# Kernel tuning notes

Measured on AMD Instinct MI355X. Metric: run time of the kernel, lower is better.

The kernel has to match this reference:

```python
import jax, jax.numpy as jnp
import numpy as np

B, D, H, P, NH = 16384, 4096, 32, 16, 32
S = H - P  # num_sub_layer = 16
TAU = 5.0
NEG = -1e9


def setup_inputs() -> dict:
    key = jax.random.key(0)
    k1, k2, k3, k4, k5 = jax.random.split(key, 5)
    x = jax.random.normal(k1, (B, D), jnp.float32)
    latency = jax.random.uniform(k2, (B,), jnp.float32)  # fraction in [0,1); clamped later
    W_head = jax.random.normal(k3, (D, S), jnp.float32) * 0.02
    b_head = jax.random.normal(k4, (S,), jnp.float32) * 0.02
    # pre-drawn gumbel noise for up to S sampling rounds: [S, B, S]
    u = jax.random.uniform(k5, (S, B, S), jnp.float32, minval=1e-6, maxval=1.0 - 1e-6)
    gumbel = -jnp.log(-jnp.log(u))
    return {"x": x, "latency": latency, "W_head": W_head, "b_head": b_head, "gumbel": gumbel}


def reference(x, latency, W_head, b_head, gumbel):
    # latency_quantizing: number of sub-layers to execute per sample
    n = jnp.clip(jnp.round(latency * H), P, H) - P  # [B] float in [0, S]
    logits = x @ W_head + b_head                    # [B, S]

    # n-times hard gumbel-softmax without replacement, vectorized over batch.
    def step(mask, inp):
        g, t = inp                                   # g: [B,S] gumbel noise, t: step index
        masked = logits + mask * NEG                 # exclude already-selected layers
        soft = jax.nn.softmax((masked + g) / TAU, axis=-1)
        hard = jax.nn.one_hot(jnp.argmax(soft, axis=-1), S, dtype=soft.dtype)
        sample = soft + jax.lax.stop_gradient(hard - soft)  # straight-through
        active = (t < n)[:, None]                    # per-sample variable draw count
        return mask + jnp.where(active, sample, 0.0), None

    ts = jnp.arange(S, dtype=jnp.float32)
    mask, _ = jax.lax.scan(step, jnp.zeros_like(logits), (gumbel, ts))  # [B, S] multi-hot

    # [B, S] -> [B, S, 2, NH]
    out = jnp.broadcast_to(mask[:, :, None, None], (mask.shape[0], S, 2, NH))
    prefix = jnp.ones((mask.shape[0], P, 2, NH), mask.dtype)  # prefix layers always run
    return jnp.concatenate([prefix, out], axis=1)             # [B, H, 2, NH]
```

## Files before the change

### kernel.cpp

```cpp
#include <hip/hip_runtime.h>


#define BB 16384
#define DD 4096

typedef float f32x4 __attribute__((ext_vector_type(4)));

__global__ __launch_bounds__(512, 2) void simple_scheduler_kernel(
    const float* __restrict__ x, const float* __restrict__ lat,
    const float* __restrict__ W, const float* __restrict__ bh,
    const float* __restrict__ gum, float* __restrict__ out) {
  __shared__ float smem[8 * 2112];

  const int t = threadIdx.x;
  const int lane = t & 63;
  const int wid = __builtin_amdgcn_readfirstlane(t >> 6);
  const int rb = blockIdx.x * 64;

  float a0[16], a1[16], a2[16], a3[16];
#pragma unroll
  for (int j = 0; j < 16; ++j) { a0[j] = 0.f; a1[j] = 0.f; a2[j] = 0.f; a3[j] = 0.f; }

  const int k0 = wid * 512;
  float* tile = smem + wid * 2112;
  const int r8 = lane >> 3;
  const int c4 = (lane & 7) * 4;
  const int lrow = lane * 33;
  const float* xbase = x + (size_t)(rb + r8) * DD + k0 + c4;

  f32x4 v[8];
#pragma unroll
  for (int rr = 0; rr < 8; ++rr)
    v[rr] = __builtin_nontemporal_load(
        reinterpret_cast<const f32x4*>(xbase + (size_t)rr * 8 * DD));

  for (int s = 0; s < 16; ++s) {
    const int kc = k0 + s * 32;
#pragma unroll
    for (int rr = 0; rr < 8; ++rr) {
      const int o = (r8 + rr * 8) * 33 + c4;
      tile[o] = v[rr].x; tile[o + 1] = v[rr].y;
      tile[o + 2] = v[rr].z; tile[o + 3] = v[rr].w;
    }
    if (s < 15) {
      const float* xn = xbase + (s + 1) * 32;
#pragma unroll
      for (int rr = 0; rr < 8; ++rr)
        v[rr] = __builtin_nontemporal_load(
            reinterpret_cast<const f32x4*>(xn + (size_t)rr * 8 * DD));
    }
#pragma unroll
    for (int i = 0; i < 32; i += 4) {
      const float x0 = tile[lrow + i];
      const float x1 = tile[lrow + i + 1];
      const float x2 = tile[lrow + i + 2];
      const float x3 = tile[lrow + i + 3];
      const float* w0 = W + (size_t)(kc + i) * 16;
#pragma unroll
      for (int j = 0; j < 16; ++j) {
        a0[j] = fmaf(w0[j],      x0, a0[j]);
        a1[j] = fmaf(w0[16 + j], x1, a1[j]);
        a2[j] = fmaf(w0[32 + j], x2, a2[j]);
        a3[j] = fmaf(w0[48 + j], x3, a3[j]);
      }
    }
  }

  __syncthreads();
  float* red    = smem;
  float* logitl = smem + 8704;
  float* selb   = smem + 9792;

#pragma unroll
  for (int j = 0; j < 16; ++j)
    red[wid * 1088 + lane * 17 + j] = (a0[j] + a1[j]) + (a2[j] + a3[j]);
  __syncthreads();

  {
    int p = t;
#pragma unroll
    for (int rep = 0; rep < 2; ++rep, p += 512) {
      const int row = p >> 4, j = p & 15;
      float ssum = 0.f;
#pragma unroll
      for (int w = 0; w < 8; ++w) ssum += red[w * 1088 + row * 17 + j];
      logitl[row * 17 + j] = ssum + bh[j];
    }
  }
  __syncthreads();

  f32x4* op = reinterpret_cast<f32x4*>(out + (size_t)rb * 2048);

  if (t >= 64) {
    const f32x4 ones = {1.f, 1.f, 1.f, 1.f};
    for (int i = t - 64; i < 64 * 256; i += 448) {
      const int row = i >> 8, col = i & 255;
      __builtin_nontemporal_store(ones, &op[(size_t)row * 512 + col]);
    }
  } else {
    const int row = rb + lane;
    float lg[16];
#pragma unroll
    for (int j = 0; j < 16; ++j) lg[j] = logitl[lane * 17 + j];

    float nf = rintf(lat[row] * 32.0f);
    nf = fminf(fmaxf(nf, 16.0f), 32.0f);
    const int n = (int)nf - 16;

    int nmax = n;
#pragma unroll
    for (int o = 32; o > 0; o >>= 1) nmax = max(nmax, __shfl_xor(nmax, o));

    unsigned sel = 0u;
    for (int tt = 0; tt < nmax; ++tt) {
      if (tt < n) {
        const float* gp = gum + ((size_t)tt * BB + row) * 16;
        const f32x4 g0 = reinterpret_cast<const f32x4*>(gp)[0];
        const f32x4 g1 = reinterpret_cast<const f32x4*>(gp)[1];
        const f32x4 g2 = reinterpret_cast<const f32x4*>(gp)[2];
        const f32x4 g3 = reinterpret_cast<const f32x4*>(gp)[3];
        const float gv[16] = {g0.x, g0.y, g0.z, g0.w, g1.x, g1.y, g1.z, g1.w,
                              g2.x, g2.y, g2.z, g2.w, g3.x, g3.y, g3.z, g3.w};
        float av[16];
#pragma unroll
        for (int j = 0; j < 16; ++j) {
          const float masked = lg[j] + (((sel >> j) & 1u) ? -1e9f : 0.0f);
          av[j] = (masked + gv[j]) / 5.0f;
        }
        float m = av[0];
#pragma unroll
        for (int j = 1; j < 16; ++j) m = fmaxf(m, av[j]);
        float ev[16];
        float se = 0.f;
#pragma unroll
        for (int j = 0; j < 16; ++j) { ev[j] = expf(av[j] - m); se += ev[j]; }
        float pm = ev[0] / se;
        int jm = 0;
#pragma unroll
        for (int j = 1; j < 16; ++j) {
          const float pj = ev[j] / se;
          if (pj > pm) { pm = pj; jm = j; }
        }
        sel |= 1u << jm;
      }
    }
#pragma unroll
    for (int j = 0; j < 16; ++j)
      selb[lane * 17 + j] = ((sel >> j) & 1u) ? 1.0f : 0.0f;
  }
  __syncthreads();

  for (int i = t; i < 64 * 256; i += 512) {
    const int row = i >> 8, c = i & 255;
    const float vv = selb[row * 17 + (c >> 4)];
    const f32x4 vvv = {vv, vv, vv, vv};
    __builtin_nontemporal_store(vvv, &op[(size_t)row * 512 + 256 + c]);
  }
}

extern "C" void kernel_launch(void* const* d_in, const int* in_sizes, int n_in,
                              void* d_out, int out_size, void* d_ws, size_t ws_size,
                              hipStream_t stream) {
  const float* x   = (const float*)d_in[0];
  const float* lat = (const float*)d_in[1];
  const float* W   = (const float*)d_in[2];
  const float* bh  = (const float*)d_in[3];
  const float* gum = (const float*)d_in[4];
  float* out = (float*)d_out;

  const int B = in_sizes[1];
  simple_scheduler_kernel<<<B / 64, 512, 0, stream>>>(x, lat, W, bh, gum, out);
}
```

Measured before the change: 442.7 us.

## Double-buffer x register prefetch and software-pipeline gumbel loads in sampling loop

The GEMV main loop now keeps two register buffers of x so loads are issued two stages ahead instead of one, giving more memory-level parallelism to hide global load latency. The gumbel-softmax sampling loop prefetches the next round's noise while computing the current round. The cost is higher register pressure (16 more f32x4 values), which under launch_bounds(512,2) could cause spills or lower occupancy.

```diff
diff --git a/kernel.cpp b/kernel.cpp
--- a/kernel.cpp
+++ b/kernel.cpp
@@ -28,43 +28,49 @@
   const int lrow = lane * 33;
   const float* xbase = x + (size_t)(rb + r8) * DD + k0 + c4;
 
-  f32x4 v[8];
+  f32x4 va[8], vb[8];
 #pragma unroll
-  for (int rr = 0; rr < 8; ++rr)
-    v[rr] = __builtin_nontemporal_load(
+  for (int rr = 0; rr < 8; ++rr) {
+    va[rr] = __builtin_nontemporal_load(
         reinterpret_cast<const f32x4*>(xbase + (size_t)rr * 8 * DD));
+    vb[rr] = __builtin_nontemporal_load(
+        reinterpret_cast<const f32x4*>(xbase + (size_t)rr * 8 * DD + 32));
+  }
 
-  for (int s = 0; s < 16; ++s) {
-    const int kc = k0 + s * 32;
-#pragma unroll
-    for (int rr = 0; rr < 8; ++rr) {
-      const int o = (r8 + rr * 8) * 33 + c4;
-      tile[o] = v[rr].x; tile[o + 1] = v[rr].y;
-      tile[o + 2] = v[rr].z; tile[o + 3] = v[rr].w;
-    }
-    if (s < 15) {
-      const float* xn = xbase + (s + 1) * 32;
-#pragma unroll
-      for (int rr = 0; rr < 8; ++rr)
-        v[rr] = __builtin_nontemporal_load(
-            reinterpret_cast<const f32x4*>(xn + (size_t)rr * 8 * DD));
-    }
-#pragma unroll
-    for (int i = 0; i < 32; i += 4) {
-      const float x0 = tile[lrow + i];
-      const float x1 = tile[lrow + i + 1];
-      const float x2 = tile[lrow + i + 2];
-      const float x3 = tile[lrow + i + 3];
-      const float* w0 = W + (size_t)(kc + i) * 16;
-#pragma unroll
-      for (int j = 0; j < 16; ++j) {
-        a0[j] = fmaf(w0[j],      x0, a0[j]);
-        a1[j] = fmaf(w0[16 + j], x1, a1[j]);
-        a2[j] = fmaf(w0[32 + j], x2, a2[j]);
-        a3[j] = fmaf(w0[48 + j], x3, a3[j]);
-      }
-    }
+#define STAGE_BODY(s, VCUR)                                                   \
+  {                                                                           \
+    const int kc = k0 + (s) * 32;                                             \
+    _Pragma("unroll") for (int rr = 0; rr < 8; ++rr) {                        \
+      const int o = (r8 + rr * 8) * 33 + c4;                                  \
+      tile[o] = VCUR[rr].x; tile[o + 1] = VCUR[rr].y;                         \
+      tile[o + 2] = VCUR[rr].z; tile[o + 3] = VCUR[rr].w;                     \
+    }                                                                         \
+    if ((s) < 14) {                                                           \
+      const float* xn = xbase + ((s) + 2) * 32;                               \
+      _Pragma("unroll") for (int rr = 0; rr < 8; ++rr)                        \
+        VCUR[rr] = __builtin_nontemporal_load(                                \
+            reinterpret_cast<const f32x4*>(xn + (size_t)rr * 8 * DD));        \
+    }                                                                         \
+    _Pragma("unroll") for (int i = 0; i < 32; i += 4) {                       \
+      const float x0 = tile[lrow + i];                                        \
+      const float x1 = tile[lrow + i + 1];                                    \
+      const float x2 = tile[lrow + i + 2];                                    \
+      const float x3 = tile[lrow + i + 3];                                    \
+      const float* w0 = W + (size_t)(kc + i) * 16;                            \
+      _Pragma("unroll") for (int j = 0; j < 16; ++j) {                        \
+        a0[j] = fmaf(w0[j],      x0, a0[j]);                                  \
+        a1[j] = fmaf(w0[16 + j], x1, a1[j]);                                  \
+        a2[j] = fmaf(w0[32 + j], x2, a2[j]);                                  \
+        a3[j] = fmaf(w0[48 + j], x3, a3[j]);                                  \
+      }                                                                       \
+    }                                                                         \
   }
+
+  for (int s = 0; s < 16; s += 2) {
+    STAGE_BODY(s, va);
+    STAGE_BODY(s + 1, vb);
+  }
+#undef STAGE_BODY
 
   __syncthreads();
   float* red    = smem;
@@ -112,36 +118,47 @@
     for (int o = 32; o > 0; o >>= 1) nmax = max(nmax, __shfl_xor(nmax, o));
 
     unsigned sel = 0u;
-    for (int tt = 0; tt < nmax; ++tt) {
-      if (tt < n) {
-        const float* gp = gum + ((size_t)tt * BB + row) * 16;
-        const f32x4 g0 = reinterpret_cast<const f32x4*>(gp)[0];
-        const f32x4 g1 = reinterpret_cast<const f32x4*>(gp)[1];
-        const f32x4 g2 = reinterpret_cast<const f32x4*>(gp)[2];
-        const f32x4 g3 = reinterpret_cast<const f32x4*>(gp)[3];
-        const float gv[16] = {g0.x, g0.y, g0.z, g0.w, g1.x, g1.y, g1.z, g1.w,
-                              g2.x, g2.y, g2.z, g2.w, g3.x, g3.y, g3.z, g3.w};
-        float av[16];
+    if (nmax > 0) {
+      const float* gb = gum + (size_t)row * 16;
+      f32x4 g0 = reinterpret_cast<const f32x4*>(gb)[0];
+      f32x4 g1 = reinterpret_cast<const f32x4*>(gb)[1];
+      f32x4 g2 = reinterpret_cast<const f32x4*>(gb)[2];
+      f32x4 g3 = reinterpret_cast<const f32x4*>(gb)[3];
+      for (int tt = 0; tt < nmax; ++tt) {
+        f32x4 h0, h1, h2, h3;
+        if (tt + 1 < nmax) {
+          const float* gp = gb + ((size_t)(tt + 1) * BB) * 16;
+          h0 = reinterpret_cast<const f32x4*>(gp)[0];
+          h1 = reinterpret_cast<const f32x4*>(gp)[1];
+          h2 = reinterpret_cast<const f32x4*>(gp)[2];
+          h3 = reinterpret_cast<const f32x4*>(gp)[3];
+        }
+        if (tt < n) {
+          const float gv[16] = {g0.x, g0.y, g0.z, g0.w, g1.x, g1.y, g1.z, g1.w,
+                                g2.x, g2.y, g2.z, g2.w, g3.x, g3.y, g3.z, g3.w};
+          float av[16];
 #pragma unroll
-        for (int j = 0; j < 16; ++j) {
-          const float masked = lg[j] + (((sel >> j) & 1u) ? -1e9f : 0.0f);
-          av[j] = (masked + gv[j]) / 5.0f;
+          for (int j = 0; j < 16; ++j) {
+            const float masked = lg[j] + (((sel >> j) & 1u) ? -1e9f : 0.0f);
+            av[j] = (masked + gv[j]) / 5.0f;
+          }
+          float m = av[0];
+#pragma unroll
+          for (int j = 1; j < 16; ++j) m = fmaxf(m, av[j]);
+          float ev[16];
+          float se = 0.f;
+#pragma unroll
+          for (int j = 0; j < 16; ++j) { ev[j] = expf(av[j] - m); se += ev[j]; }
+          float pm = ev[0] / se;
+          int jm = 0;
+#pragma unroll
+          for (int j = 1; j < 16; ++j) {
+            const float pj = ev[j] / se;
+            if (pj > pm) { pm = pj; jm = j; }
+          }
+          sel |= 1u << jm;
         }
-        float m = av[0];
-#pragma unroll
-        for (int j = 1; j < 16; ++j) m = fmaxf(m, av[j]);
-        float ev[16];
-        float se = 0.f;
-#pragma unroll
-        for (int j = 0; j < 16; ++j) { ev[j] = expf(av[j] - m); se += ev[j]; }
-        float pm = ev[0] / se;
-        int jm = 0;
-#pragma unroll
-        for (int j = 1; j < 16; ++j) {
-          const float pj = ev[j] / se;
-          if (pj > pm) { pm = pj; jm = j; }
-        }
-        sel |= 1u << jm;
+        g0 = h0; g1 = h1; g2 = h2; g3 = h3;
       }
     }
 #pragma unroll
```

Result: slower. 501.1 us (+13.2%).

## Double block to 1024 threads, split K-slices across wave pairs, prefetch gumbel rows

Applied to the files above, without the earlier changes.

Each block now runs 16 waves instead of 8. Pairs of waves share a 512-wide K slice, each handling two of every four columns with float2 loads, and the reduction sums 16 partial buffers. This halves accumulator registers per thread, raises the number of loads in flight and aims to hide x-stream latency better. The gumbel sampling loop also prefetches the next step's noise row ahead of the softmax compute. In exchange, x loads become narrower 8-byte accesses and the cross-wave reduction gets longer.

```diff
diff --git a/kernel.cpp b/kernel.cpp
--- a/kernel.cpp
+++ b/kernel.cpp
@@ -5,87 +5,87 @@
 #define DD 4096
 
 typedef float f32x4 __attribute__((ext_vector_type(4)));
+typedef float f32x2 __attribute__((ext_vector_type(2)));
 
-__global__ __launch_bounds__(512, 2) void simple_scheduler_kernel(
+__global__ __launch_bounds__(1024, 4) void simple_scheduler_kernel(
     const float* __restrict__ x, const float* __restrict__ lat,
     const float* __restrict__ W, const float* __restrict__ bh,
     const float* __restrict__ gum, float* __restrict__ out) {
-  __shared__ float smem[8 * 2112];
+  __shared__ float smem[16 * 1088];
 
   const int t = threadIdx.x;
   const int lane = t & 63;
   const int wid = __builtin_amdgcn_readfirstlane(t >> 6);
   const int rb = blockIdx.x * 64;
 
-  float a0[16], a1[16], a2[16], a3[16];
+  const int kpart = wid & 7;
+  const int k0 = kpart * 512;
+  const int hs = (wid >= 8) ? 2 : 0;
+
+  float a0[16], a1[16];
 #pragma unroll
-  for (int j = 0; j < 16; ++j) { a0[j] = 0.f; a1[j] = 0.f; a2[j] = 0.f; a3[j] = 0.f; }
+  for (int j = 0; j < 16; ++j) { a0[j] = 0.f; a1[j] = 0.f; }
 
-  const int k0 = wid * 512;
-  float* tile = smem + wid * 2112;
+  float* tile = smem + wid * 1088;
   const int r8 = lane >> 3;
-  const int c4 = (lane & 7) * 4;
-  const int lrow = lane * 33;
-  const float* xbase = x + (size_t)(rb + r8) * DD + k0 + c4;
+  const int c = lane & 7;
+  const int lrow = lane * 17;
+  const float* xbase = x + (size_t)(rb + r8) * DD + k0 + 4 * c + hs;
+  const float* wbase = W + hs * 16;
 
-  f32x4 v[8];
+  f32x2 v[8];
 #pragma unroll
   for (int rr = 0; rr < 8; ++rr)
     v[rr] = __builtin_nontemporal_load(
-        reinterpret_cast<const f32x4*>(xbase + (size_t)rr * 8 * DD));
+        reinterpret_cast<const f32x2*>(xbase + (size_t)rr * 8 * DD));
 
   for (int s = 0; s < 16; ++s) {
-    const int kc = k0 + s * 32;
 #pragma unroll
     for (int rr = 0; rr < 8; ++rr) {
-      const int o = (r8 + rr * 8) * 33 + c4;
+      const int o = (r8 + rr * 8) * 17 + 2 * c;
       tile[o] = v[rr].x; tile[o + 1] = v[rr].y;
-      tile[o + 2] = v[rr].z; tile[o + 3] = v[rr].w;
     }
     if (s < 15) {
       const float* xn = xbase + (s + 1) * 32;
 #pragma unroll
       for (int rr = 0; rr < 8; ++rr)
         v[rr] = __builtin_nontemporal_load(
-            reinterpret_cast<const f32x4*>(xn + (size_t)rr * 8 * DD));
+            reinterpret_cast<const f32x2*>(xn + (size_t)rr * 8 * DD));
     }
 #pragma unroll
-    for (int i = 0; i < 32; i += 4) {
-      const float x0 = tile[lrow + i];
-      const float x1 = tile[lrow + i + 1];
-      const float x2 = tile[lrow + i + 2];
-      const float x3 = tile[lrow + i + 3];
-      const float* w0 = W + (size_t)(kc + i) * 16;
+    for (int i = 0; i < 8; ++i) {
+      const float x0 = tile[lrow + 2 * i];
+      const float x1 = tile[lrow + 2 * i + 1];
+      const float* w0 = wbase + (size_t)(k0 + s * 32 + 4 * i) * 16;
 #pragma unroll
       for (int j = 0; j < 16; ++j) {
         a0[j] = fmaf(w0[j],      x0, a0[j]);
         a1[j] = fmaf(w0[16 + j], x1, a1[j]);
-        a2[j] = fmaf(w0[32 + j], x2, a2[j]);
-        a3[j] = fmaf(w0[48 + j], x3, a3[j]);
       }
     }
   }
 
   __syncthreads();
-  float* red    = smem;
-  float* logitl = smem + 8704;
-  float* selb   = smem + 9792;
+  float* red = smem;
 
 #pragma unroll
   for (int j = 0; j < 16; ++j)
-    red[wid * 1088 + lane * 17 + j] = (a0[j] + a1[j]) + (a2[j] + a3[j]);
+    red[wid * 1088 + lane * 17 + j] = a0[j] + a1[j];
   __syncthreads();
 
+  float* logitl = smem;
+  float* selb   = smem + 1088;
   {
-    int p = t;
+    const int row = t >> 4, j = t & 15;
+    float ssum = 0.f;
 #pragma unroll
-    for (int rep = 0; rep < 2; ++rep, p += 512) {
-      const int row = p >> 4, j = p & 15;
-      float ssum = 0.f;
-#pragma unroll
-      for (int w = 0; w < 8; ++w) ssum += red[w * 1088 + row * 17 + j];
-      logitl[row * 17 + j] = ssum + bh[j];
+    for (int w = 0; w < 8; ++w) {
+      const float pr = red[w * 1088 + row * 17 + j] +
+                       red[(w + 8) * 1088 + row * 17 + j];
+      ssum += pr;
     }
+    const float lv = ssum + bh[j];
+    logitl[row * 17 + j] = lv;
   }
   __syncthreads();
 
@@ -93,7 +93,7 @@
 
   if (t >= 64) {
     const f32x4 ones = {1.f, 1.f, 1.f, 1.f};
-    for (int i = t - 64; i < 64 * 256; i += 448) {
+    for (int i = t - 64; i < 64 * 256; i += 960) {
       const int row = i >> 8, col = i & 255;
       __builtin_nontemporal_store(ones, &op[(size_t)row * 512 + col]);
     }
@@ -112,36 +112,47 @@
     for (int o = 32; o > 0; o >>= 1) nmax = max(nmax, __shfl_xor(nmax, o));
 
     unsigned sel = 0u;
-    for (int tt = 0; tt < nmax; ++tt) {
-      if (tt < n) {
-        const float* gp = gum + ((size_t)tt * BB + row) * 16;
-        const f32x4 g0 = reinterpret_cast<const f32x4*>(gp)[0];
-        const f32x4 g1 = reinterpret_cast<const f32x4*>(gp)[1];
-        const f32x4 g2 = reinterpret_cast<const f32x4*>(gp)[2];
-        const f32x4 g3 = reinterpret_cast<const f32x4*>(gp)[3];
-        const float gv[16] = {g0.x, g0.y, g0.z, g0.w, g1.x, g1.y, g1.z, g1.w,
-                              g2.x, g2.y, g2.z, g2.w, g3.x, g3.y, g3.z, g3.w};
-        float av[16];
+    if (nmax > 0) {
+      const float* gb = gum + (size_t)row * 16;
+      f32x4 g0 = reinterpret_cast<const f32x4*>(gb)[0];
+      f32x4 g1 = reinterpret_cast<const f32x4*>(gb)[1];
+      f32x4 g2 = reinterpret_cast<const f32x4*>(gb)[2];
+      f32x4 g3 = reinterpret_cast<const f32x4*>(gb)[3];
+      for (int tt = 0; tt < nmax; ++tt) {
+        f32x4 h0, h1, h2, h3;
+        if (tt + 1 < nmax) {
+          const float* gp = gb + ((size_t)(tt + 1) * BB) * 16;
+          h0 = reinterpret_cast<const f32x4*>(gp)[0];
+          h1 = reinterpret_cast<const f32x4*>(gp)[1];
+          h2 = reinterpret_cast<const f32x4*>(gp)[2];
+          h3 = reinterpret_cast<const f32x4*>(gp)[3];
+        }
+        if (tt < n) {
+          const float gv[16] = {g0.x, g0.y, g0.z, g0.w, g1.x, g1.y, g1.z, g1.w,
+                                g2.x, g2.y, g2.z, g2.w, g3.x, g3.y, g3.z, g3.w};
+          float av[16];
 #pragma unroll
-        for (int j = 0; j < 16; ++j) {
-          const float masked = lg[j] + (((sel >> j) & 1u) ? -1e9f : 0.0f);
-          av[j] = (masked + gv[j]) / 5.0f;
+          for (int j = 0; j < 16; ++j) {
+            const float masked = lg[j] + (((sel >> j) & 1u) ? -1e9f : 0.0f);
+            av[j] = (masked + gv[j]) / 5.0f;
+          }
+          float m = av[0];
+#pragma unroll
+          for (int j = 1; j < 16; ++j) m = fmaxf(m, av[j]);
+          float ev[16];
+          float se = 0.f;
+#pragma unroll
+          for (int j = 0; j < 16; ++j) { ev[j] = expf(av[j] - m); se += ev[j]; }
+          float pm = ev[0] / se;
+          int jm = 0;
+#pragma unroll
+          for (int j = 1; j < 16; ++j) {
+            const float pj = ev[j] / se;
+            if (pj > pm) { pm = pj; jm = j; }
+          }
+          sel |= 1u << jm;
         }
-        float m = av[0];
-#pragma unroll
-        for (int j = 1; j < 16; ++j) m = fmaxf(m, av[j]);
-        float ev[16];
-        float se = 0.f;
-#pragma unroll
-        for (int j = 0; j < 16; ++j) { ev[j] = expf(av[j] - m); se += ev[j]; }
-        float pm = ev[0] / se;
-        int jm = 0;
-#pragma unroll
-        for (int j = 1; j < 16; ++j) {
-          const float pj = ev[j] / se;
-          if (pj > pm) { pm = pj; jm = j; }
-        }
-        sel |= 1u << jm;
+        g0 = h0; g1 = h1; g2 = h2; g3 = h3;
       }
     }
 #pragma unroll
@@ -150,11 +161,11 @@
   }
   __syncthreads();
 
-  for (int i = t; i < 64 * 256; i += 512) {
-    const int row = i >> 8, c = i & 255;
-    const float vv = selb[row * 17 + (c >> 4)];
+  for (int i = t; i < 64 * 256; i += 1024) {
+    const int row = i >> 8, cc = i & 255;
+    const float vv = selb[row * 17 + (cc >> 4)];
     const f32x4 vvv = {vv, vv, vv, vv};
-    __builtin_nontemporal_store(vvv, &op[(size_t)row * 512 + 256 + c]);
+    __builtin_nontemporal_store(vvv, &op[(size_t)row * 512 + 256 + cc]);
   }
 }
 
@@ -169,5 +180,5 @@
   float* out = (float*)d_out;
 
   const int B = in_sizes[1];
-  simple_scheduler_kernel<<<B / 64, 512, 0, stream>>>(x, lat, W, bh, gum, out);
+  simple_scheduler_kernel<<<B / 64, 1024, 0, stream>>>(x, lat, W, bh, gum, out);
 }
```

After: 454.1 us. 2.6% more time.
